# Kernel tuning notes

Measured on AMD Instinct MI355X. Metric: run time of the kernel, lower is better.

## Reference

```python
import jax, jax.numpy as jnp
import numpy as np

B, S, D, H, DK = 2, 2048, 1024, 16, 64
NUM_BUCKETS, MAX_DIST = 32, 128
EPS = 1e-6


def _relative_position_bucket(rel, num_buckets=NUM_BUCKETS, max_distance=MAX_DIST):
    # bidirectional (T5 encoder) bucketing
    nb = num_buckets // 2
    bucket = (rel > 0).astype(jnp.int32) * nb
    n = jnp.abs(rel)
    max_exact = nb // 2
    is_small = n < max_exact
    large = max_exact + (
        jnp.log(jnp.maximum(n, 1).astype(jnp.float32) / max_exact)
        / np.log(max_distance / max_exact)
        * (nb - max_exact)
    ).astype(jnp.int32)
    large = jnp.minimum(large, nb - 1)
    return bucket + jnp.where(is_small, n, large)


def softmax1(logits):
    # off-by-one softmax: exp(x-m) / (sum(exp(x-m)) + exp(-m))
    m = jax.lax.stop_gradient(jnp.max(logits, axis=-1, keepdims=True))
    e = jnp.exp(logits - m)
    return e / (jnp.sum(e, axis=-1, keepdims=True) + jnp.exp(-m))


def setup_inputs() -> dict:
    key = jax.random.key(0)
    ks = jax.random.split(key, 8)
    scale = 0.02
    return {
        "hidden_states": jax.random.normal(ks[0], (B, S, D), dtype=jnp.float32),
        "delete_gate_mask": jax.random.normal(ks[1], (B, S, 1), dtype=jnp.float32),
        "ln_w": jnp.ones((D,), dtype=jnp.float32),
        "q_w": jax.random.normal(ks[2], (D, H * DK), dtype=jnp.float32) * scale,
        "k_w": jax.random.normal(ks[3], (D, H * DK), dtype=jnp.float32) * scale,
        "v_w": jax.random.normal(ks[4], (D, H * DK), dtype=jnp.float32) * scale,
        "o_w": jax.random.normal(ks[5], (H * DK, D), dtype=jnp.float32) * scale,
        "rel_emb": jax.random.normal(ks[6], (NUM_BUCKETS, H), dtype=jnp.float32) * scale,
    }


def reference(hidden_states, delete_gate_mask, ln_w, q_w, k_w, v_w, o_w, rel_emb):
    # T5LayerNorm (RMS norm, no mean subtraction, no bias)
    var = jnp.mean(jnp.square(hidden_states), axis=-1, keepdims=True)
    x = hidden_states * jax.lax.rsqrt(var + EPS) * ln_w

    # projections (T5 Linear layers have no bias, no 1/sqrt(d) scaling)
    q = (x @ q_w).reshape(B, S, H, DK).transpose(0, 2, 1, 3)  # bhqd
    k = (x @ k_w).reshape(B, S, H, DK).transpose(0, 2, 1, 3)  # bhkd
    v = (x @ v_w).reshape(B, S, H, DK).transpose(0, 2, 1, 3)  # bhkd

    scores = jnp.einsum("bhqd,bhkd->bhqk", q, k)

    # relative position bias: [1, H, S, S]
    pos = jnp.arange(S)
    rel = pos[None, :] - pos[:, None]  # key_pos - query_pos
    bucket = _relative_position_bucket(rel)  # [S, S]
    position_bias = rel_emb[bucket].transpose(2, 0, 1)[None]  # [1,H,S,S]

    # delete gate: [B,S,1] -> additive mask over key axis [B,1,1,S]
    gate = delete_gate_mask[..., 0][:, None, None, :]

    scores = scores + position_bias + gate
    attn = softmax1(scores.astype(jnp.float32)).astype(scores.dtype)

    attn_out = jnp.einsum("bhqk,bhkd->bhqd", attn, v)
    attn_out = attn_out.transpose(0, 2, 1, 3).reshape(B, S, H * DK) @ o_w

    # residual (dropout disabled at p=0)
    return hidden_states + attn_out
```

## Files before the change

kernel.cpp:

```cpp
#include <hip/hip_runtime.h>
#include <hip/hip_bf16.h>
#include <math.h>

typedef __attribute__((ext_vector_type(8))) short short8;
typedef __attribute__((ext_vector_type(4))) float f32x4;

#define S_LEN   2048
#define DMODEL  1024
#define NHEAD   16
#define HDK     64
#define NBATCH  2
#define MTOT    (NBATCH*S_LEN)
#define LOG2E   1.4426950408889634f

__device__ __forceinline__ unsigned short f2bf(float f) {
  union { float f; unsigned u; } c; c.f = f;
  unsigned r = c.u + 0x7FFFu + ((c.u >> 16) & 1u);
  return (unsigned short)(r >> 16);
}

__device__ __forceinline__ short8 lds_ld16(const unsigned short* p) {
  return *reinterpret_cast<const short8*>(p);
}

__device__ __forceinline__ void gload_lds16(const unsigned short* g, unsigned short* l) {
  __builtin_amdgcn_global_load_lds(
      (const __attribute__((address_space(1))) unsigned int*)g,
      (__attribute__((address_space(3))) unsigned int*)l, 16, 0, 0);
}

__global__ __launch_bounds__(256) void transpose_w_kernel(
    const float* __restrict__ qw, const float* __restrict__ kw,
    const float* __restrict__ vw, const float* __restrict__ ow,
    unsigned short* __restrict__ wqkv, unsigned short* __restrict__ wo) {
  int z = blockIdx.z;
  const float* src = (z==0)?qw:(z==1)?kw:(z==2)?vw:ow;
  unsigned short* dst = (z<3) ? (wqkv + (size_t)z*DMODEL*DMODEL) : wo;
  __shared__ float tile[32][33];
  int n0 = blockIdx.x*32, k0 = blockIdx.y*32;
  int tx = threadIdx.x, ty = threadIdx.y;
  for (int r = ty; r < 32; r += 8)
    tile[r][tx] = src[(size_t)(k0+r)*DMODEL + n0 + tx];
  __syncthreads();
  for (int r = ty; r < 32; r += 8)
    dst[(size_t)(n0+r)*DMODEL + k0 + tx] = f2bf(tile[tx][r]);
}

__global__ void bias_table_kernel(const float* __restrict__ rel_emb,
                                  float* __restrict__ btab) {
  int idx = blockIdx.x*256 + threadIdx.x;
  if (idx >= NHEAD*4095) return;
  int h = idx / 4095, rp = idx % 4095, rel = rp - 2047;
  int bucket = (rel > 0) ? 16 : 0;
  int n = (rel < 0) ? -rel : rel;
  int v;
  if (n < 8) v = n;
  else {
    float lrv = logf((float)n * 0.125f) / 2.7725887f * 8.0f;
    v = 8 + (int)lrv;
    if (v > 15) v = 15;
  }
  btab[idx] = rel_emb[(size_t)(bucket + v)*NHEAD + h] * LOG2E;
}

__global__ void eg_kernel(const float* __restrict__ gmask,
                          float* __restrict__ egf,
                          unsigned short* __restrict__ egb) {
  int i = blockIdx.x*256 + threadIdx.x;
  float e = __expf(gmask[i]);
  egf[i] = e;
  egb[i] = f2bf(e);
}

__global__ __launch_bounds__(256) void rmsnorm_kernel(
    const float* __restrict__ hs, const float* __restrict__ lnw,
    unsigned short* __restrict__ xo) {
  int row = blockIdx.x, t = threadIdx.x;
  const float4 v = ((const float4*)(hs + (size_t)row*DMODEL))[t];
  float ss = v.x*v.x + v.y*v.y + v.z*v.z + v.w*v.w;
  #pragma unroll
  for (int off = 32; off >= 1; off >>= 1) ss += __shfl_xor(ss, off, 64);
  __shared__ float wsum[4];
  if ((t & 63) == 0) wsum[t >> 6] = ss;
  __syncthreads();
  float tot = wsum[0] + wsum[1] + wsum[2] + wsum[3];
  float sc = rsqrtf(tot * (1.0f/DMODEL) + 1e-6f);
  const float4 lw = ((const float4*)lnw)[t];
  uint2 o;
  o.x = (unsigned)f2bf(v.x*sc*lw.x) | ((unsigned)f2bf(v.y*sc*lw.y) << 16);
  o.y = (unsigned)f2bf(v.z*sc*lw.z) | ((unsigned)f2bf(v.w*sc*lw.w) << 16);
  ((uint2*)(xo + (size_t)row*DMODEL))[t] = o;
}

template<int EPI>
__global__ __launch_bounds__(256) void gemm128(
    const unsigned short* __restrict__ X,
    const unsigned short* __restrict__ W,
    unsigned short* __restrict__ Oq, unsigned short* __restrict__ Ok,
    unsigned short* __restrict__ Ov,
    const float* __restrict__ resid, float* __restrict__ Of,
    const float* __restrict__ escale) {
  __shared__ unsigned short As[128*64];
  __shared__ unsigned short Bs[128*64];
  const int z = blockIdx.z;
  int m0, n0;
  const unsigned short *Ap, *Bp;
  if (EPI == 0 && z == 2) {
    m0 = blockIdx.y*128; n0 = blockIdx.x*128;
    Ap = W + (size_t)2*DMODEL*DMODEL; Bp = X;
  } else {
    m0 = blockIdx.x*128; n0 = blockIdx.y*128;
    Ap = X; Bp = W + ((EPI==0) ? (size_t)z*DMODEL*DMODEL : 0);
  }
  const int t = threadIdx.x, lane = t & 63, w = t >> 6;
  const int g = lane >> 4, lr = lane & 15;
  const int wr = (w >> 1)*64, wc = (w & 1)*64;

  f32x4 acc[4][4];
  #pragma unroll
  for (int mi = 0; mi < 4; mi++)
    #pragma unroll
    for (int ni = 0; ni < 4; ni++) acc[mi][ni] = (f32x4){0.f,0.f,0.f,0.f};

  const unsigned short* ag[4]; const unsigned short* bg[4];
  unsigned short* al[4]; unsigned short* bl[4];
  #pragma unroll
  for (int i = 0; i < 4; i++) {
    int slot = t + i*256, row = slot >> 3, c8 = slot & 7;
    int cs = c8 ^ (row & 7);
    ag[i] = Ap + (size_t)(m0 + row)*DMODEL + cs*8;
    bg[i] = Bp + (size_t)(n0 + row)*DMODEL + cs*8;
    al[i] = As + slot*8;
    bl[i] = Bs + slot*8;
  }

  for (int kk = 0; kk < DMODEL; kk += 64) {
    #pragma unroll
    for (int i = 0; i < 4; i++) {
      gload_lds16(ag[i] + kk, al[i]);
      gload_lds16(bg[i] + kk, bl[i]);
    }
    __syncthreads();
    #pragma unroll
    for (int ks = 0; ks < 2; ks++) {
      short8 af[4], bfr[4];
      #pragma unroll
      for (int mi = 0; mi < 4; mi++) {
        int R = wr + mi*16 + lr;
        af[mi] = lds_ld16(As + R*64 + (((ks*4 + g) ^ (R & 7)) << 3));
      }
      #pragma unroll
      for (int ni = 0; ni < 4; ni++) {
        int R = wc + ni*16 + lr;
        bfr[ni] = lds_ld16(Bs + R*64 + (((ks*4 + g) ^ (R & 7)) << 3));
      }
      #pragma unroll
      for (int mi = 0; mi < 4; mi++)
        #pragma unroll
        for (int ni = 0; ni < 4; ni++)
          acc[mi][ni] = __builtin_amdgcn_mfma_f32_16x16x32_bf16(af[mi], bfr[ni], acc[mi][ni], 0, 0, 0);
    }
    __syncthreads();
  }

  if (EPI == 0) {
    if (z < 2) {
      unsigned short* dst = (z == 0) ? Oq : Ok;
      const float osc = (z == 0) ? LOG2E : 1.0f;
      #pragma unroll
      for (int mi = 0; mi < 4; mi++) {
        #pragma unroll
        for (int r = 0; r < 4; r++) {
          int m = m0 + wr + mi*16 + g*4 + r;
          int b = m >> 11, s = m & (S_LEN-1);
          unsigned short* drow = dst + ((size_t)b*NHEAD*S_LEN + s)*HDK;
          #pragma unroll
          for (int ni = 0; ni < 4; ni++) {
            int n = n0 + wc + ni*16 + lr;
            int h = n >> 6, dcol = n & 63;
            drow[(size_t)h*S_LEN*HDK + dcol] = f2bf(acc[mi][ni][r] * osc);
          }
        }
      }
    } else {
      #pragma unroll
      for (int ni = 0; ni < 4; ni++) {
        int n = n0 + wc + ni*16 + lr;
        int b = n >> 11, s = n & (S_LEN-1);
        float e = escale[n];
        #pragma unroll
        for (int mi = 0; mi < 4; mi++)
          #pragma unroll
          for (int r = 0; r < 4; r++) {
            int m = m0 + wr + mi*16 + g*4 + r;
            Ov[((size_t)b*DMODEL + m)*S_LEN + s] = f2bf(acc[mi][ni][r] * e);
          }
      }
    }
  } else {
    #pragma unroll
    for (int mi = 0; mi < 4; mi++) {
      #pragma unroll
      for (int r = 0; r < 4; r++) {
        int m = m0 + wr + mi*16 + g*4 + r;
        const float* rrow = resid + (size_t)m*DMODEL;
        float* orow = Of + (size_t)m*DMODEL;
        #pragma unroll
        for (int ni = 0; ni < 4; ni++) {
          int n = n0 + wc + ni*16 + lr;
          orow[n] = rrow[n] + acc[mi][ni][r];
        }
      }
    }
  }
}

__global__ __launch_bounds__(256, 2) void attn_kernel(
    const unsigned short* __restrict__ Qg,
    const unsigned short* __restrict__ Kg,
    const unsigned short* __restrict__ Vtg,
    const float* __restrict__ btab,
    const unsigned short* __restrict__ egb,
    unsigned short* __restrict__ Og) {
  __shared__ __align__(16) unsigned short Kl[2][128*64];
  __shared__ __align__(16) unsigned short Vl[2][64*128];
  __shared__ __align__(16) unsigned short Pl[4][2][16*64];

  const int flat = blockIdx.x;
  const int xcd = flat & 7, j = flat >> 3;
  const int bh = xcd*4 + (j >> 4), qx = j & 15;
  const int b = bh >> 4, h = bh & 15;
  const int q0 = qx * 128;

  const int t = threadIdx.x, w = t >> 6, lane = t & 63;
  const int g = lane >> 4, lr = lane & 15, l7 = lane & 7;

  const unsigned short* Qb = Qg  + (size_t)bh*S_LEN*HDK;
  const unsigned short* Kb = Kg  + (size_t)bh*S_LEN*HDK;
  const unsigned short* Vb = Vtg + (size_t)bh*HDK*S_LEN;
  const unsigned short* ge = egb + (size_t)b*S_LEN;

  const unsigned short* kS[4]; const unsigned short* vS[4]; int so[4];
  #pragma unroll
  for (int i = 0; i < 4; i++) {
    int slot = t + i*256; so[i] = slot*8;
    int krow = slot >> 3, kg = slot & 7;
    kS[i] = Kb + (size_t)krow*HDK + ((kg ^ (krow & 7)) << 3);
    int vrow = slot >> 4, vg = slot & 15;
    int vcs = (vg & 8) | ((vg & 7) ^ (vrow & 7));
    vS[i] = Vb + (size_t)vrow*S_LEN + vcs*8;
  }
#define STAGE(nb_, key_) do {                                          \
    _Pragma("unroll") for (int i = 0; i < 4; i++) {                    \
      gload_lds16(kS[i] + (size_t)(key_)*HDK, &Kl[nb_][0] + so[i]);    \
      gload_lds16(vS[i] + (key_),             &Vl[nb_][0] + so[i]);    \
    } } while (0)

  const int qs0A = q0 + w*32, qs0B = qs0A + 16;
  short8 qfA0 = *reinterpret_cast<const short8*>(Qb + (size_t)(qs0A+lr)*HDK + g*8);
  short8 qfA1 = *reinterpret_cast<const short8*>(Qb + (size_t)(qs0A+lr)*HDK + 32 + g*8);
  short8 qfB0 = *reinterpret_cast<const short8*>(Qb + (size_t)(qs0B+lr)*HDK + g*8);
  short8 qfB1 = *reinterpret_cast<const short8*>(Qb + (size_t)(qs0B+lr)*HDK + 32 + g*8);

  f32x4 accA[4], accB[4], l4A, l4B;
  #pragma unroll
  for (int n = 0; n < 4; n++) { accA[n] = (f32x4){0.f,0.f,0.f,0.f}; accB[n] = (f32x4){0.f,0.f,0.f,0.f}; }
  l4A = (f32x4){0.f,0.f,0.f,0.f}; l4B = (f32x4){0.f,0.f,0.f,0.f};

  const float* btb = btab + (size_t)h*4095 + 2047;
  const float cpos = btb[91];
  const float cneg = btb[-91];

  char* prowA = (char*)&Pl[w][0][0] + lr*128;
  char* prowB = (char*)&Pl[w][1][0] + lr*128;

  STAGE(0, 0);
  int cur = 0;
  for (int kt = 0; kt < S_LEN/128; ++kt) {
    const int key0 = kt*128;
    __syncthreads();

    if (kt + 1 < S_LEN/128) STAGE(cur^1, key0+128);

    #pragma unroll
    for (int hh = 0; hh < 2; hh++) {
      const int k64 = key0 + hh*64;
      const unsigned short* Klh = &Kl[cur][0] + hh*64*64;

      short8 gvh[2];
      #pragma unroll
      for (int c = 0; c < 2; c++) {
        short8 z8 = (short8){0,0,0,0,0,0,0,0};
        if (lr == 0)
          z8 = *reinterpret_cast<const short8*>(ge + k64 + c*32 + g*8);
        gvh[c] = z8;
      }

      const int dbA = k64 - qs0A, dbB = k64 - qs0B;
      const bool bandA = (dbA > -154 && dbA < 106);
      const bool bandB = (dbB > -154 && dbB < 106);
      const float ccA = bandA ? 0.f : ((dbA > 0) ? cpos : cneg);
      const float ccB = bandB ? 0.f : ((dbB > 0) ? cpos : cneg);
      f32x4 svA[4], svB[4];
      {
        f32x4 zA = (f32x4){ccA,ccA,ccA,ccA}, zB = (f32x4){ccB,ccB,ccB,ccB};
        short8 bk[4];
        #pragma unroll
        for (int n = 0; n < 4; n++)
          bk[n] = lds_ld16(Klh + (n*16 + lr)*64 + ((g ^ l7) << 3));
        __builtin_amdgcn_s_setprio(1);
        #pragma unroll
        for (int n = 0; n < 4; n++) {
          svA[n] = __builtin_amdgcn_mfma_f32_16x16x32_bf16(bk[n], qfA0, zA, 0, 0, 0);
          svB[n] = __builtin_amdgcn_mfma_f32_16x16x32_bf16(bk[n], qfB0, zB, 0, 0, 0);
        }
        __builtin_amdgcn_s_setprio(0);
        #pragma unroll
        for (int n = 0; n < 4; n++)
          bk[n] = lds_ld16(Klh + (n*16 + lr)*64 + (((4 + g) ^ l7) << 3));
        __builtin_amdgcn_s_setprio(1);
        #pragma unroll
        for (int n = 0; n < 4; n++) {
          svA[n] = __builtin_amdgcn_mfma_f32_16x16x32_bf16(bk[n], qfA1, svA[n], 0, 0, 0);
          svB[n] = __builtin_amdgcn_mfma_f32_16x16x32_bf16(bk[n], qfB1, svB[n], 0, 0, 0);
        }
        __builtin_amdgcn_s_setprio(0);
      }

#define FINISH_SM(sv_, band_, db_, prow_)                                             \
      {                                                                               \
        if (band_) {                                                                  \
          const float* btq = btb + ((db_) - lr);                                      \
          _Pragma("unroll") for (int n = 0; n < 4; n++)                               \
            _Pragma("unroll") for (int r = 0; r < 4; r++)                             \
              sv_[n][r] += btq[n*16 + g*4 + r];                                       \
        }                                                                             \
        _Pragma("unroll") for (int n = 0; n < 4; n++)                                 \
          _Pragma("unroll") for (int r = 0; r < 4; r++)                               \
            sv_[n][r] = exp2f(sv_[n][r]);                                             \
        _Pragma("unroll") for (int n = 0; n < 4; n++) {                               \
          unsigned plo_, phi_;                                                        \
          asm("v_cvt_pk_bf16_f32 %0, %1, %2" : "=v"(plo_) : "v"(sv_[n][0]), "v"(sv_[n][1])); \
          asm("v_cvt_pk_bf16_f32 %0, %1, %2" : "=v"(phi_) : "v"(sv_[n][2]), "v"(sv_[n][3])); \
          uint2 pw_; pw_.x = plo_; pw_.y = phi_;                                      \
          *reinterpret_cast<uint2*>((prow_) + ((((2*n + (g>>1)) ^ l7) << 4) + ((g & 1) << 3))) = pw_; \
        }                                                                             \
      }
      FINISH_SM(svA, bandA, dbA, prowA)
      FINISH_SM(svB, bandB, dbB, prowB)
#undef FINISH_SM

      #pragma unroll
      for (int c = 0; c < 2; c++) {
        int gr = hh*8 + c*4 + g;
        int grs = (gr & 8) | ((gr & 7) ^ l7);
        short8 bvf[4];
        #pragma unroll
        for (int n = 0; n < 4; n++)
          bvf[n] = lds_ld16(&Vl[cur][0] + (n*16 + lr)*128 + grs*8);
        short8 paA = lds_ld16((const unsigned short*)(prowA + (((4*c + g) ^ l7) << 4)));
        short8 paB = lds_ld16((const unsigned short*)(prowB + (((4*c + g) ^ l7) << 4)));
        __builtin_amdgcn_s_setprio(1);
        #pragma unroll
        for (int n = 0; n < 4; n++) {
          accA[n] = __builtin_amdgcn_mfma_f32_16x16x32_bf16(paA, bvf[n], accA[n], 0, 0, 0);
          accB[n] = __builtin_amdgcn_mfma_f32_16x16x32_bf16(paB, bvf[n], accB[n], 0, 0, 0);
        }
        l4A = __builtin_amdgcn_mfma_f32_16x16x32_bf16(paA, gvh[c], l4A, 0, 0, 0);
        l4B = __builtin_amdgcn_mfma_f32_16x16x32_bf16(paB, gvh[c], l4B, 0, 0, 0);
        __builtin_amdgcn_s_setprio(0);
      }
    }

    cur ^= 1;
  }

#define FINAL_SET(acc_, l4_, qs0_)                                                    \
  {                                                                                   \
    _Pragma("unroll") for (int r = 0; r < 4; r++) {                                   \
      float lq = __shfl(l4_[r], g*16);                                                \
      float inv = 1.0f / (lq + 1.0f);                                                 \
      int srw = (qs0_) + g*4 + r;                                                     \
      unsigned short* orow = Og + ((size_t)b*S_LEN + srw)*DMODEL + h*HDK;             \
      _Pragma("unroll") for (int n = 0; n < 4; n++)                                   \
        orow[n*16 + lr] = f2bf(acc_[n][r] * inv);                                     \
    }                                                                                 \
  }
  FINAL_SET(accA, l4A, qs0A)
  FINAL_SET(accB, l4B, qs0B)
#undef FINAL_SET
#undef STAGE
}

extern "C" void kernel_launch(void* const* d_in, const int* in_sizes, int n_in,
                              void* d_out, int out_size, void* d_ws, size_t ws_size,
                              hipStream_t stream) {
  const float* hs   = (const float*)d_in[0];
  const float* gate = (const float*)d_in[1];
  const float* lnw  = (const float*)d_in[2];
  const float* qw   = (const float*)d_in[3];
  const float* kw   = (const float*)d_in[4];
  const float* vw   = (const float*)d_in[5];
  const float* ow   = (const float*)d_in[6];
  const float* rel  = (const float*)d_in[7];
  float* out = (float*)d_out;

  char* ws = (char*)d_ws;
  const size_t MB = 1ull << 20;
  unsigned short* xbf  = (unsigned short*)(ws);
  unsigned short* wqkv = (unsigned short*)(ws + 8*MB);
  unsigned short* wo   = (unsigned short*)(ws + 14*MB);
  unsigned short* qb   = (unsigned short*)(ws + 16*MB);
  unsigned short* kb   = (unsigned short*)(ws + 24*MB);
  unsigned short* vt   = (unsigned short*)(ws + 32*MB);
  unsigned short* ao   = (unsigned short*)(ws + 40*MB);
  float*          btab = (float*)(ws + 48*MB);
  float*          egf  = (float*)(ws + 48*MB + 256*1024);
  unsigned short* egb  = (unsigned short*)(ws + 48*MB + 272*1024);

  transpose_w_kernel<<<dim3(32,32,4), dim3(32,8), 0, stream>>>(qw, kw, vw, ow, wqkv, wo);
  bias_table_kernel<<<dim3(256), dim3(256), 0, stream>>>(rel, btab);
  eg_kernel<<<dim3(16), dim3(256), 0, stream>>>(gate, egf, egb);
  rmsnorm_kernel<<<dim3(MTOT), dim3(256), 0, stream>>>(hs, lnw, xbf);
  gemm128<0><<<dim3(MTOT/128, DMODEL/128, 3), dim3(256), 0, stream>>>(
      xbf, wqkv, qb, kb, vt, nullptr, nullptr, egf);
  attn_kernel<<<dim3(512), dim3(256), 0, stream>>>(
      qb, kb, vt, btab, egb, ao);
  gemm128<1><<<dim3(MTOT/128, DMODEL/128, 1), dim3(256), 0, stream>>>(
      ao, wo, nullptr, nullptr, nullptr, hs, out, nullptr);
}
```

Baseline: 140.3 us.

## Switch attention to 32x32x16 MFMA and keep P in registers via permlane swap

The attention kernel's 16x16x32 MFMA tiles are replaced with 32x32x16 tiles over 32-key sub-blocks. The softmax probability tile is rearranged in registers with v_permlane32_swap instead of being written to and read back from LDS, so the per-wave P buffer is gone. This removes LDS traffic and instruction overhead per tile. The costs are more accumulator registers, which may lower occupancy, and the gate vector is now loaded by every lane rather than one lane per row group.

```diff
diff --git a/kernel.cpp b/kernel.cpp
--- a/kernel.cpp
+++ b/kernel.cpp
@@ -4,6 +4,7 @@
 
 typedef __attribute__((ext_vector_type(8))) short short8;
 typedef __attribute__((ext_vector_type(4))) float f32x4;
+typedef __attribute__((ext_vector_type(16))) float f32x16;
 
 #define S_LEN   2048
 #define DMODEL  1024
@@ -224,7 +225,6 @@
     unsigned short* __restrict__ Og) {
   __shared__ __align__(16) unsigned short Kl[2][128*64];
   __shared__ __align__(16) unsigned short Vl[2][64*128];
-  __shared__ __align__(16) unsigned short Pl[4][2][16*64];
 
   const int flat = blockIdx.x;
   const int xcd = flat & 7, j = flat >> 3;
@@ -233,7 +233,7 @@
   const int q0 = qx * 128;
 
   const int t = threadIdx.x, w = t >> 6, lane = t & 63;
-  const int g = lane >> 4, lr = lane & 15, l7 = lane & 7;
+  const int col = lane & 31, hi = lane >> 5;
 
   const unsigned short* Qb = Qg  + (size_t)bh*S_LEN*HDK;
   const unsigned short* Kb = Kg  + (size_t)bh*S_LEN*HDK;
@@ -256,23 +256,19 @@
       gload_lds16(vS[i] + (key_),             &Vl[nb_][0] + so[i]);    \
     } } while (0)
 
-  const int qs0A = q0 + w*32, qs0B = qs0A + 16;
-  short8 qfA0 = *reinterpret_cast<const short8*>(Qb + (size_t)(qs0A+lr)*HDK + g*8);
-  short8 qfA1 = *reinterpret_cast<const short8*>(Qb + (size_t)(qs0A+lr)*HDK + 32 + g*8);
-  short8 qfB0 = *reinterpret_cast<const short8*>(Qb + (size_t)(qs0B+lr)*HDK + g*8);
-  short8 qfB1 = *reinterpret_cast<const short8*>(Qb + (size_t)(qs0B+lr)*HDK + 32 + g*8);
-
-  f32x4 accA[4], accB[4], l4A, l4B;
-  #pragma unroll
-  for (int n = 0; n < 4; n++) { accA[n] = (f32x4){0.f,0.f,0.f,0.f}; accB[n] = (f32x4){0.f,0.f,0.f,0.f}; }
-  l4A = (f32x4){0.f,0.f,0.f,0.f}; l4B = (f32x4){0.f,0.f,0.f,0.f};
+  const int qw0 = q0 + w*32;
+  short8 qf[4];
+  #pragma unroll
+  for (int kk = 0; kk < 4; kk++)
+    qf[kk] = *reinterpret_cast<const short8*>(Qb + (size_t)(qw0 + col)*HDK + kk*16 + hi*8);
+
+  f32x16 oacc0, oacc1, l4;
+  #pragma unroll
+  for (int r = 0; r < 16; r++) { oacc0[r] = 0.f; oacc1[r] = 0.f; l4[r] = 0.f; }
 
   const float* btb = btab + (size_t)h*4095 + 2047;
   const float cpos = btb[91];
   const float cneg = btb[-91];
-
-  char* prowA = (char*)&Pl[w][0][0] + lr*128;
-  char* prowB = (char*)&Pl[w][1][0] + lr*128;
 
   STAGE(0, 0);
   int cur = 0;
@@ -283,112 +279,75 @@
     if (kt + 1 < S_LEN/128) STAGE(cur^1, key0+128);
 
     #pragma unroll
-    for (int hh = 0; hh < 2; hh++) {
-      const int k64 = key0 + hh*64;
-      const unsigned short* Klh = &Kl[cur][0] + hh*64*64;
-
-      short8 gvh[2];
-      #pragma unroll
-      for (int c = 0; c < 2; c++) {
-        short8 z8 = (short8){0,0,0,0,0,0,0,0};
-        if (lr == 0)
-          z8 = *reinterpret_cast<const short8*>(ge + k64 + c*32 + g*8);
-        gvh[c] = z8;
-      }
-
-      const int dbA = k64 - qs0A, dbB = k64 - qs0B;
-      const bool bandA = (dbA > -154 && dbA < 106);
-      const bool bandB = (dbB > -154 && dbB < 106);
-      const float ccA = bandA ? 0.f : ((dbA > 0) ? cpos : cneg);
-      const float ccB = bandB ? 0.f : ((dbB > 0) ? cpos : cneg);
-      f32x4 svA[4], svB[4];
+    for (int kb = 0; kb < 4; kb++) {
+      const int k32 = key0 + kb*32;
+      const int db = k32 - qw0;
+      const bool farp = (db >= 122), farn = (db <= -122);
+      const float cc = farp ? cpos : (farn ? cneg : 0.f);
+
+      f32x16 sv;
       {
-        f32x4 zA = (f32x4){ccA,ccA,ccA,ccA}, zB = (f32x4){ccB,ccB,ccB,ccB};
-        short8 bk[4];
-        #pragma unroll
-        for (int n = 0; n < 4; n++)
-          bk[n] = lds_ld16(Klh + (n*16 + lr)*64 + ((g ^ l7) << 3));
+        f32x16 zc;
+        #pragma unroll
+        for (int r = 0; r < 16; r++) zc[r] = cc;
+        const unsigned short* krow = &Kl[cur][(size_t)(kb*32 + col)*64];
+        const int ksw = (kb*32 + col) & 7;
         __builtin_amdgcn_s_setprio(1);
         #pragma unroll
-        for (int n = 0; n < 4; n++) {
-          svA[n] = __builtin_amdgcn_mfma_f32_16x16x32_bf16(bk[n], qfA0, zA, 0, 0, 0);
-          svB[n] = __builtin_amdgcn_mfma_f32_16x16x32_bf16(bk[n], qfB0, zB, 0, 0, 0);
+        for (int kk = 0; kk < 4; kk++) {
+          short8 ka = lds_ld16(krow + (((hi + 2*kk) ^ ksw) << 3));
+          sv = __builtin_amdgcn_mfma_f32_32x32x16_bf16(ka, qf[kk], kk ? sv : zc, 0, 0, 0);
         }
         __builtin_amdgcn_s_setprio(0);
-        #pragma unroll
-        for (int n = 0; n < 4; n++)
-          bk[n] = lds_ld16(Klh + (n*16 + lr)*64 + (((4 + g) ^ l7) << 3));
+      }
+
+      if (!farp && !farn) {
+        const float* btq = btb + (db - col) + 4*hi;
+        #pragma unroll
+        for (int r = 0; r < 16; r++)
+          sv[r] += btq[(r & 3) + 8*(r >> 2)];
+      }
+
+      #pragma unroll
+      for (int r = 0; r < 16; r++) sv[r] = exp2f(sv[r]);
+      unsigned pk[8];
+      #pragma unroll
+      for (int jj = 0; jj < 8; jj++)
+        asm("v_cvt_pk_bf16_f32 %0, %1, %2" : "=v"(pk[jj]) : "v"(sv[2*jj]), "v"(sv[2*jj+1]));
+      asm("v_permlane32_swap_b32 %0, %1" : "+v"(pk[0]), "+v"(pk[2]));
+      asm("v_permlane32_swap_b32 %0, %1" : "+v"(pk[1]), "+v"(pk[3]));
+      asm("v_permlane32_swap_b32 %0, %1" : "+v"(pk[4]), "+v"(pk[6]));
+      asm("v_permlane32_swap_b32 %0, %1" : "+v"(pk[5]), "+v"(pk[7]));
+      union { unsigned u[4]; short8 s; } pa0c, pa1c;
+      pa0c.u[0] = pk[0]; pa0c.u[1] = pk[1]; pa0c.u[2] = pk[2]; pa0c.u[3] = pk[3];
+      pa1c.u[0] = pk[4]; pa1c.u[1] = pk[5]; pa1c.u[2] = pk[6]; pa1c.u[3] = pk[7];
+
+      #pragma unroll
+      for (int ck = 0; ck < 2; ck++) {
+        short8 pa = ck ? pa1c.s : pa0c.s;
+        int grv = kb*4 + ck*2 + hi;
+        int swv = (grv & 8) | ((grv & 7) ^ (col & 7));
+        short8 bv0 = lds_ld16(&Vl[cur][(size_t)col*128 + swv*8]);
+        short8 bv1 = lds_ld16(&Vl[cur][(size_t)(col+32)*128 + swv*8]);
+        short8 egf8 = *reinterpret_cast<const short8*>(ge + k32 + ck*16 + hi*8);
         __builtin_amdgcn_s_setprio(1);
-        #pragma unroll
-        for (int n = 0; n < 4; n++) {
-          svA[n] = __builtin_amdgcn_mfma_f32_16x16x32_bf16(bk[n], qfA1, svA[n], 0, 0, 0);
-          svB[n] = __builtin_amdgcn_mfma_f32_16x16x32_bf16(bk[n], qfB1, svB[n], 0, 0, 0);
-        }
+        oacc0 = __builtin_amdgcn_mfma_f32_32x32x16_bf16(pa, bv0, oacc0, 0, 0, 0);
+        oacc1 = __builtin_amdgcn_mfma_f32_32x32x16_bf16(pa, bv1, oacc1, 0, 0, 0);
+        l4    = __builtin_amdgcn_mfma_f32_32x32x16_bf16(pa, egf8, l4, 0, 0, 0);
         __builtin_amdgcn_s_setprio(0);
       }
-
-#define FINISH_SM(sv_, band_, db_, prow_)                                             \
-      {                                                                               \
-        if (band_) {                                                                  \
-          const float* btq = btb + ((db_) - lr);                                      \
-          _Pragma("unroll") for (int n = 0; n < 4; n++)                               \
-            _Pragma("unroll") for (int r = 0; r < 4; r++)                             \
-              sv_[n][r] += btq[n*16 + g*4 + r];                                       \
-        }                                                                             \
-        _Pragma("unroll") for (int n = 0; n < 4; n++)                                 \
-          _Pragma("unroll") for (int r = 0; r < 4; r++)                               \
-            sv_[n][r] = exp2f(sv_[n][r]);                                             \
-        _Pragma("unroll") for (int n = 0; n < 4; n++) {                               \
-          unsigned plo_, phi_;                                                        \
-          asm("v_cvt_pk_bf16_f32 %0, %1, %2" : "=v"(plo_) : "v"(sv_[n][0]), "v"(sv_[n][1])); \
-          asm("v_cvt_pk_bf16_f32 %0, %1, %2" : "=v"(phi_) : "v"(sv_[n][2]), "v"(sv_[n][3])); \
-          uint2 pw_; pw_.x = plo_; pw_.y = phi_;                                      \
-          *reinterpret_cast<uint2*>((prow_) + ((((2*n + (g>>1)) ^ l7) << 4) + ((g & 1) << 3))) = pw_; \
-        }                                                                             \
-      }
-      FINISH_SM(svA, bandA, dbA, prowA)
-      FINISH_SM(svB, bandB, dbB, prowB)
-#undef FINISH_SM
-
-      #pragma unroll
-      for (int c = 0; c < 2; c++) {
-        int gr = hh*8 + c*4 + g;
-        int grs = (gr & 8) | ((gr & 7) ^ l7);
-        short8 bvf[4];
-        #pragma unroll
-        for (int n = 0; n < 4; n++)
-          bvf[n] = lds_ld16(&Vl[cur][0] + (n*16 + lr)*128 + grs*8);
-        short8 paA = lds_ld16((const unsigned short*)(prowA + (((4*c + g) ^ l7) << 4)));
-        short8 paB = lds_ld16((const unsigned short*)(prowB + (((4*c + g) ^ l7) << 4)));
-        __builtin_amdgcn_s_setprio(1);
-        #pragma unroll
-        for (int n = 0; n < 4; n++) {
-          accA[n] = __builtin_amdgcn_mfma_f32_16x16x32_bf16(paA, bvf[n], accA[n], 0, 0, 0);
-          accB[n] = __builtin_amdgcn_mfma_f32_16x16x32_bf16(paB, bvf[n], accB[n], 0, 0, 0);
-        }
-        l4A = __builtin_amdgcn_mfma_f32_16x16x32_bf16(paA, gvh[c], l4A, 0, 0, 0);
-        l4B = __builtin_amdgcn_mfma_f32_16x16x32_bf16(paB, gvh[c], l4B, 0, 0, 0);
-        __builtin_amdgcn_s_setprio(0);
-      }
-    }
-
+    }
     cur ^= 1;
   }
 
-#define FINAL_SET(acc_, l4_, qs0_)                                                    \
-  {                                                                                   \
-    _Pragma("unroll") for (int r = 0; r < 4; r++) {                                   \
-      float lq = __shfl(l4_[r], g*16);                                                \
-      float inv = 1.0f / (lq + 1.0f);                                                 \
-      int srw = (qs0_) + g*4 + r;                                                     \
-      unsigned short* orow = Og + ((size_t)b*S_LEN + srw)*DMODEL + h*HDK;             \
-      _Pragma("unroll") for (int n = 0; n < 4; n++)                                   \
-        orow[n*16 + lr] = f2bf(acc_[n][r] * inv);                                     \
-    }                                                                                 \
-  }
-  FINAL_SET(accA, l4A, qs0A)
-  FINAL_SET(accB, l4B, qs0B)
-#undef FINAL_SET
+  #pragma unroll
+  for (int r = 0; r < 16; r++) {
+    float inv = 1.0f / (l4[r] + 1.0f);
+    int q = qw0 + (r & 3) + 8*(r >> 2) + 4*hi;
+    unsigned short* orow = Og + ((size_t)b*S_LEN + q)*DMODEL + h*HDK;
+    orow[col]      = f2bf(oacc0[r] * inv);
+    orow[col + 32] = f2bf(oacc1[r] * inv);
+  }
 #undef STAGE
 }
 
```

New measurement: 142.4 us. About the same (+1.5%).
